# Performance work log

Measured on AMD Instinct MI355X. Metric: run time of the kernel, lower is better.

Reference implementation:

```python
import jax, jax.numpy as jnp
import numpy as np

N = 8192
D = 512


def setup_inputs() -> dict:
    key = jax.random.key(0)
    ks = jax.random.split(key, 7)
    X = jax.random.normal(ks[0], (N, D), dtype=jnp.float32)
    adj = jax.random.randint(ks[1], (N, N), 0, 2, dtype=jnp.int32)
    # guarantee at least one neighbor per row (self-loop) so softmax is defined
    adj = adj.at[jnp.arange(N), jnp.arange(N)].set(1)
    s = 1.0 / np.sqrt(D)
    Wq = jax.random.normal(ks[2], (D, D), dtype=jnp.float32) * s
    Wk = jax.random.normal(ks[3], (D, D), dtype=jnp.float32) * s
    Wv = jax.random.normal(ks[4], (D, D), dtype=jnp.float32) * s
    Wo = jax.random.normal(ks[5], (D, D), dtype=jnp.float32) * s
    bo = jnp.zeros((D,), dtype=jnp.float32)
    return {"X": X, "adj": adj, "Wq": Wq, "Wk": Wk, "Wv": Wv, "Wo": Wo, "bo": bo}


def reference(X, adj, Wq, Wk, Wv, Wo, bo):
    # torch Linear(no bias): y = x @ W.T
    Q = X @ Wq.T                                  # [N, D]
    K = X @ Wk.T                                  # [N, D]
    V = X @ Wv.T                                  # [N, D]
    scale = 1.0 / jnp.sqrt(jnp.asarray(D, X.dtype))
    scores = jnp.einsum('nd,md->nm', Q, K) * scale  # [N, N]
    scores = jnp.where(adj == 0, -jnp.inf, scores)
    attn = jax.nn.softmax(scores, axis=-1)          # [N, N]
    out = attn @ V                                  # [N, D]
    out = out @ Wo.T + bo                           # [N, D]
    return out
```

## Files before the change

### kernel.cpp

```cpp
#include <hip/hip_runtime.h>

namespace {

constexpr int NR = 8192;
constexpr int DD = 512;
constexpr int NSPLIT = 4;
constexpr int KVLEN = NR / NSPLIT;
constexpr int KT = 32;
constexpr int NT = KVLEN / KT;
constexpr int QB = 64;
constexpr float SCALE = 0.04419417382415922f;

typedef __bf16 bf16x8 __attribute__((ext_vector_type(8)));
typedef __bf16 bf16x4 __attribute__((ext_vector_type(4)));
typedef float  f32x16 __attribute__((ext_vector_type(16)));

__device__ __forceinline__ f32x16 mfma(bf16x8 a, bf16x8 b, f32x16 c) {
    return __builtin_amdgcn_mfma_f32_32x32x16_bf16(a, b, c, 0, 0, 0);
}

__device__ __forceinline__ size_t kfa(int n, int d) {
    size_t chunk = (size_t)(((n >> 5) * 4 + (d >> 7)) * 8 + ((d >> 4) & 7));
    return chunk * 512 + ((((d >> 3) & 1) * 32 + (n & 31)) * 8) + (d & 7);
}
__device__ __forceinline__ size_t vfa(int n, int d) {
    size_t chunk = (size_t)(((n >> 5) * 4 + (d >> 7)) * 8 +
                            ((d >> 6) & 1) * 4 + ((d >> 5) & 1) * 2 + ((n >> 4) & 1));
    return chunk * 512 + ((((n >> 3) & 1) * 32 + (d & 31)) * 8) + (n & 7);
}

__global__ void __launch_bounds__(256)
cast_kernel(const float* __restrict__ in, __bf16* __restrict__ out, int n8) {
    int i = blockIdx.x * 256 + threadIdx.x;
    if (i >= n8) return;
    const float4* p = (const float4*)(in + (size_t)i * 8);
    float4 v0 = p[0], v1 = p[1];
    bf16x8 o;
    o[0] = (__bf16)v0.x; o[1] = (__bf16)v0.y; o[2] = (__bf16)v0.z; o[3] = (__bf16)v0.w;
    o[4] = (__bf16)v1.x; o[5] = (__bf16)v1.y; o[6] = (__bf16)v1.z; o[7] = (__bf16)v1.w;
    *(bf16x8*)(out + (size_t)i * 8) = o;
}

__global__ void __launch_bounds__(256)
bitpack_kernel(const int* __restrict__ adj, unsigned long long* __restrict__ abits) {
    const int w = threadIdx.x >> 6, lane = threadIdx.x & 63;
    const int q = blockIdx.x * 4 + w;
    const int* row = adj + (size_t)q * NR;
    unsigned long long* orow = abits + (size_t)q * (NR / 64);
    for (int i = 0; i < NR / 64; ++i) {
        unsigned long long m = __ballot(row[i * 64 + lane] != 0);
        if (lane == 0) orow[i] = m;
    }
}

template<bool FINAL>
__global__ void __launch_bounds__(256, 2)
gemm_kernel(const __bf16* __restrict__ A, const __bf16* __restrict__ B0,
            const __bf16* __restrict__ B1, const __bf16* __restrict__ B2,
            __bf16* __restrict__ C0, __bf16* __restrict__ C1, __bf16* __restrict__ C2,
            const float* __restrict__ bias, float* __restrict__ Cf)
{
    const __bf16* B = B0;
    __bf16* Cb = C0;
    int mode = 0;
    if (!FINAL) {
        if (blockIdx.y == 1)      { B = B1; Cb = C1; mode = 1; }
        else if (blockIdx.y == 2) { B = B2; Cb = C2; mode = 2; }
    }
    __shared__ __bf16 As[128][72];
    __shared__ __bf16 Bs[128][72];
    const int t = threadIdx.x;
    const int w = t >> 6, lane = t & 63, lo = lane & 31, hi = lane >> 5;
    const int wm = w >> 1, wn = w & 1;
    const int bm = (blockIdx.x >> 2) * 128;
    const int bn = (blockIdx.x & 3) * 128;

    f32x16 acc[2][2];
    #pragma unroll
    for (int a = 0; a < 2; ++a)
        #pragma unroll
        for (int b = 0; b < 2; ++b)
            #pragma unroll
            for (int r = 0; r < 16; ++r) acc[a][b][r] = 0.f;

    for (int k0 = 0; k0 < DD; k0 += 64) {
        __syncthreads();
        #pragma unroll
        for (int pp = 0; pp < 2; ++pp) {
            int r = pp * 64 + (t >> 2), c = (t & 3) * 16;
            *(bf16x8*)&As[r][c]     = *(const bf16x8*)(A + (size_t)(bm + r) * DD + k0 + c);
            *(bf16x8*)&As[r][c + 8] = *(const bf16x8*)(A + (size_t)(bm + r) * DD + k0 + c + 8);
            *(bf16x8*)&Bs[r][c]     = *(const bf16x8*)(B + (size_t)(bn + r) * DD + k0 + c);
            *(bf16x8*)&Bs[r][c + 8] = *(const bf16x8*)(B + (size_t)(bn + r) * DD + k0 + c + 8);
        }
        __syncthreads();
        #pragma unroll
        for (int ks = 0; ks < 4; ++ks) {
            bf16x8 a0 = *(const bf16x8*)&As[wm * 64 + lo][ks * 16 + hi * 8];
            bf16x8 a1 = *(const bf16x8*)&As[wm * 64 + 32 + lo][ks * 16 + hi * 8];
            bf16x8 b0 = *(const bf16x8*)&Bs[wn * 64 + lo][ks * 16 + hi * 8];
            bf16x8 b1 = *(const bf16x8*)&Bs[wn * 64 + 32 + lo][ks * 16 + hi * 8];
            acc[0][0] = mfma(a0, b0, acc[0][0]);
            acc[0][1] = mfma(a0, b1, acc[0][1]);
            acc[1][0] = mfma(a1, b0, acc[1][0]);
            acc[1][1] = mfma(a1, b1, acc[1][1]);
        }
    }
    #pragma unroll
    for (int mi = 0; mi < 2; ++mi)
        #pragma unroll
        for (int ni = 0; ni < 2; ++ni) {
            int col = bn + wn * 64 + ni * 32 + lo;
            float bv = 0.f;
            if (FINAL) bv = bias[col];
            #pragma unroll
            for (int r = 0; r < 16; ++r) {
                int row = bm + wm * 64 + mi * 32 + (r & 3) + 8 * (r >> 2) + 4 * hi;
                if (FINAL) {
                    Cf[(size_t)row * DD + col] = acc[mi][ni][r] + bv;
                } else {
                    size_t a;
                    if (mode == 1)      a = kfa(row, col);
                    else if (mode == 2) a = vfa(row, col);
                    else                a = (size_t)row * DD + col;
                    Cb[a] = (__bf16)acc[mi][ni][r];
                }
            }
        }
}

__global__ void __launch_bounds__(256, 2)
flash_kernel(const __bf16* __restrict__ Qg, const __bf16* __restrict__ KF,
             const __bf16* __restrict__ VF, const unsigned long long* __restrict__ abits,
             __bf16* __restrict__ Opart, float* __restrict__ lsum_g)
{
    __shared__ __bf16 Sp[4][QB][40];
    __shared__ __bf16 Pl[QB][40];
    __shared__ float  ll[QB];

    const int t = threadIdx.x;
    const int w = t >> 6, lane = t & 63, lo = lane & 31, hi = lane >> 5;
    const int bid = blockIdx.x;
    const int xcd = bid & 7;
    const int split = xcd >> 1;
    const int qblk = (((xcd & 1) << 6) | (bid >> 3)) * QB;
    const int kv0 = split * KVLEN;

    bf16x8 qa[2][8];
    #pragma unroll
    for (int mi = 0; mi < 2; ++mi)
        #pragma unroll
        for (int ks = 0; ks < 8; ++ks)
            qa[mi][ks] = *(const bf16x8*)(Qg + (size_t)(qblk + mi * 32 + lo) * DD + w * 128 + ks * 16 + hi * 8);

    f32x16 O[2][2][2];
    #pragma unroll
    for (int h = 0; h < 2; ++h)
        #pragma unroll
        for (int a = 0; a < 2; ++a)
            #pragma unroll
            for (int b = 0; b < 2; ++b)
                #pragma unroll
                for (int r = 0; r < 16; ++r) O[h][a][b][r] = 0.f;

    const int qo = w * 16 + (lane >> 2);
    const int c8 = (lane & 3) * 8;
    const unsigned long long* abp = abits + (size_t)(qblk + qo) * (NR / 64) + kv0 / 64;
    unsigned long long acur = abp[0];
    unsigned long long anxt = abp[1];

    float l_run = 0.f;

    for (int tl = 0; tl < NT; ++tl) {
        if (tl && !(tl & 1)) {
            acur = anxt;
            int idx = (tl >> 1) + 1; if (idx > 31) idx = 31;
            anxt = abp[idx];
        }
        const int tile = (kv0 >> 5) + tl;
        const __bf16* kf = KF + (size_t)(tile * 4 + w) * 4096;

        f32x16 St0, St1;
        #pragma unroll
        for (int r = 0; r < 16; ++r) { St0[r] = 0.f; St1[r] = 0.f; }
        #pragma unroll
        for (int ks = 0; ks < 8; ++ks) {
            bf16x8 kb = *(const bf16x8*)(kf + ks * 512 + lane * 8);
            St0 = mfma(kb, qa[0][ks], St0);
            St1 = mfma(kb, qa[1][ks], St1);
        }
        #pragma unroll
        for (int g = 0; g < 4; ++g) {
            bf16x4 v0, v1;
            #pragma unroll
            for (int j = 0; j < 4; ++j) { v0[j] = (__bf16)St0[4 * g + j]; v1[j] = (__bf16)St1[4 * g + j]; }
            *(bf16x4*)&Sp[w][lo][8 * g + 4 * hi]      = v0;
            *(bf16x4*)&Sp[w][32 + lo][8 * g + 4 * hi] = v1;
        }
        __syncthreads();

        {
            bf16x8 p0 = *(const bf16x8*)&Sp[0][qo][c8];
            bf16x8 p1 = *(const bf16x8*)&Sp[1][qo][c8];
            bf16x8 p2 = *(const bf16x8*)&Sp[2][qo][c8];
            bf16x8 p3 = *(const bf16x8*)&Sp[3][qo][c8];
            unsigned m8 = ((unsigned)(acur >> ((tl & 1) << 5)) >> c8) & 0xffu;
            float lsum = 0.f;
            bf16x8 pb;
            #pragma unroll
            for (int i = 0; i < 8; ++i) {
                float v = ((float)p0[i] + (float)p1[i] + (float)p2[i] + (float)p3[i]) * SCALE;
                float pv = ((m8 >> i) & 1u) ? __expf(v) : 0.f;
                lsum += pv;
                pb[i] = (__bf16)pv;
            }
            lsum += __shfl_xor(lsum, 1);
            lsum += __shfl_xor(lsum, 2);
            l_run += lsum;
            *(bf16x8*)&Pl[qo][c8] = pb;
        }
        __syncthreads();

        bf16x8 pa[2][2];
        #pragma unroll
        for (int mi = 0; mi < 2; ++mi)
            #pragma unroll
            for (int ks = 0; ks < 2; ++ks)
                pa[mi][ks] = *(const bf16x8*)&Pl[mi * 32 + lo][ks * 16 + hi * 8];
        const __bf16* vf = VF + (size_t)(tile * 4 + w) * 4096;
        #pragma unroll
        for (int h = 0; h < 2; ++h)
            #pragma unroll
            for (int ni = 0; ni < 2; ++ni) {
                bf16x8 vb0 = *(const bf16x8*)(vf + (h * 4 + ni * 2 + 0) * 512 + lane * 8);
                bf16x8 vb1 = *(const bf16x8*)(vf + (h * 4 + ni * 2 + 1) * 512 + lane * 8);
                O[h][0][ni] = mfma(pa[0][0], vb0, O[h][0][ni]);
                O[h][1][ni] = mfma(pa[1][0], vb0, O[h][1][ni]);
                O[h][0][ni] = mfma(pa[0][1], vb1, O[h][0][ni]);
                O[h][1][ni] = mfma(pa[1][1], vb1, O[h][1][ni]);
            }
    }
    if ((lane & 3) == 0) {
        ll[qo] = l_run;
        lsum_g[(size_t)split * NR + qblk + qo] = l_run;
    }
    __syncthreads();
    #pragma unroll
    for (int mi = 0; mi < 2; ++mi)
        #pragma unroll
        for (int g = 0; g < 4; ++g) {
            float4 lv = *(const float4*)&ll[mi * 32 + 8 * g + 4 * hi];
            #pragma unroll
            for (int j = 0; j < 4; ++j) {
                float lval = (&lv.x)[j];
                float inv = (lval > 0.f) ? 1.f / lval : 0.f;
                int row = qblk + mi * 32 + 8 * g + 4 * hi + j;
                #pragma unroll
                for (int h = 0; h < 2; ++h)
                    #pragma unroll
                    for (int ni = 0; ni < 2; ++ni) {
                        int col = w * 128 + h * 64 + ni * 32 + lo;
                        Opart[(size_t)split * NR * DD + (size_t)row * DD + col] =
                            (__bf16)(O[h][mi][ni][g * 4 + j] * inv);
                    }
            }
        }
}

__global__ void __launch_bounds__(256)
merge_kernel(const __bf16* __restrict__ Opart, const float* __restrict__ lsum_g,
             __bf16* __restrict__ attn)
{
    int idx = blockIdx.x * 256 + threadIdx.x;
    int q = idx >> 6;
    int c = (idx & 63) * 8;
    float l0 = lsum_g[q], l1 = lsum_g[NR + q], l2 = lsum_g[2 * NR + q], l3 = lsum_g[3 * NR + q];
    float Winv = 1.f / (l0 + l1 + l2 + l3);
    float w0 = l0 * Winv, w1 = l1 * Winv, w2 = l2 * Winv, w3 = l3 * Winv;
    const size_t base = (size_t)q * DD + c;
    const size_t stride = (size_t)NR * DD;
    bf16x8 o0 = *(const bf16x8*)(Opart + base);
    bf16x8 o1 = *(const bf16x8*)(Opart + stride + base);
    bf16x8 o2 = *(const bf16x8*)(Opart + 2 * stride + base);
    bf16x8 o3 = *(const bf16x8*)(Opart + 3 * stride + base);
    bf16x8 o;
    #pragma unroll
    for (int i = 0; i < 8; ++i)
        o[i] = (__bf16)(w0 * (float)o0[i] + w1 * (float)o1[i] +
                        w2 * (float)o2[i] + w3 * (float)o3[i]);
    *(bf16x8*)(attn + base) = o;
}

}

extern "C" void kernel_launch(void* const* d_in, const int* in_sizes, int n_in,
                              void* d_out, int out_size, void* d_ws, size_t ws_size,
                              hipStream_t stream)
{
    (void)in_sizes; (void)n_in; (void)out_size; (void)ws_size;
    const float* X  = (const float*)d_in[0];
    const int*   adj = (const int*)d_in[1];
    const float* Wq = (const float*)d_in[2];
    const float* Wk = (const float*)d_in[3];
    const float* Wv = (const float*)d_in[4];
    const float* Wo = (const float*)d_in[5];
    const float* bo = (const float*)d_in[6];
    float* out = (float*)d_out;

    char* ws = (char*)d_ws;
    __bf16* Xb   = (__bf16*)(ws + 0);
    __bf16* Att  = (__bf16*)(ws + 0);
    __bf16* Wqb  = (__bf16*)(ws + 8388608);
    __bf16* Wkb  = (__bf16*)(ws + 8912896);
    __bf16* Wvb  = (__bf16*)(ws + 9437184);
    __bf16* Wob  = (__bf16*)(ws + 9961472);
    __bf16* Qb   = (__bf16*)(ws + 10485760);
    __bf16* KFb  = (__bf16*)(ws + 18874368);
    __bf16* VFb  = (__bf16*)(ws + 27262976);
    unsigned long long* abits = (unsigned long long*)(ws + 35651584);
    __bf16* Op   = (__bf16*)(ws + 44040192);
    float*  lseb = (float*)(ws + 77594624);

    bitpack_kernel<<<2048, 256, 0, stream>>>(adj, abits);
    cast_kernel<<<2048, 256, 0, stream>>>(X,  Xb,  NR * DD / 8);
    cast_kernel<<<128,  256, 0, stream>>>(Wq, Wqb, DD * DD / 8);
    cast_kernel<<<128,  256, 0, stream>>>(Wk, Wkb, DD * DD / 8);
    cast_kernel<<<128,  256, 0, stream>>>(Wv, Wvb, DD * DD / 8);
    cast_kernel<<<128,  256, 0, stream>>>(Wo, Wob, DD * DD / 8);

    gemm_kernel<false><<<dim3(256, 3), 256, 0, stream>>>(Xb, Wqb, Wkb, Wvb,
                                                         Qb, KFb, VFb, nullptr, nullptr);
    flash_kernel<<<512, 256, 0, stream>>>(Qb, KFb, VFb, abits, Op, lseb);
    merge_kernel<<<2048, 256, 0, stream>>>(Op, lseb, Att);
    gemm_kernel<true><<<dim3(256, 1), 256, 0, stream>>>(Att, Wob, nullptr, nullptr,
                                                        nullptr, nullptr, nullptr, bo, out);
}
```

Before: 459.8 us.

## Software-pipeline flash loop and repack V in a separate transpose kernel

```diff
diff --git a/kernel.cpp b/kernel.cpp
--- a/kernel.cpp
+++ b/kernel.cpp
@@ -65,7 +65,7 @@
     int mode = 0;
     if (!FINAL) {
         if (blockIdx.y == 1)      { B = B1; Cb = C1; mode = 1; }
-        else if (blockIdx.y == 2) { B = B2; Cb = C2; mode = 2; }
+        else if (blockIdx.y == 2) { B = B2; Cb = C2; }
     }
     __shared__ __bf16 As[128][72];
     __shared__ __bf16 Bs[128][72];
@@ -119,14 +119,35 @@
                 if (FINAL) {
                     Cf[(size_t)row * DD + col] = acc[mi][ni][r] + bv;
                 } else {
-                    size_t a;
-                    if (mode == 1)      a = kfa(row, col);
-                    else if (mode == 2) a = vfa(row, col);
-                    else                a = (size_t)row * DD + col;
+                    size_t a = (mode == 1) ? kfa(row, col) : ((size_t)row * DD + col);
                     Cb[a] = (__bf16)acc[mi][ni][r];
                 }
             }
         }
+}
+
+__global__ void __launch_bounds__(256)
+repack_v(const __bf16* __restrict__ V, __bf16* __restrict__ VF) {
+    __shared__ __bf16 tile[64][72];
+    const int t = threadIdx.x;
+    const int rb = blockIdx.x * 64;
+    const int cb = blockIdx.y * 64;
+    #pragma unroll
+    for (int pp = 0; pp < 2; ++pp) {
+        int r = pp * 32 + (t >> 3), c = (t & 7) * 8;
+        *(bf16x8*)&tile[r][c] = *(const bf16x8*)(V + (size_t)(rb + r) * DD + cb + c);
+    }
+    __syncthreads();
+    #pragma unroll
+    for (int pp = 0; pp < 2; ++pp) {
+        int vid = pp * 256 + t;
+        int oct = vid >> 6;
+        int dd = vid & 63;
+        bf16x8 o;
+        #pragma unroll
+        for (int e = 0; e < 8; ++e) o[e] = tile[oct * 8 + e][dd];
+        *(bf16x8*)(VF + vfa(rb + oct * 8, cb + dd)) = o;
+    }
 }
 
 __global__ void __launch_bounds__(256, 2)
@@ -170,16 +191,10 @@
     unsigned long long anxt = abp[1];
 
     float l_run = 0.f;
-
-    for (int tl = 0; tl < NT; ++tl) {
-        if (tl && !(tl & 1)) {
-            acur = anxt;
-            int idx = (tl >> 1) + 1; if (idx > 31) idx = 31;
-            anxt = abp[idx];
-        }
-        const int tile = (kv0 >> 5) + tl;
-        const __bf16* kf = KF + (size_t)(tile * 4 + w) * 4096;
-
+    const int tile0 = kv0 >> 5;
+
+    {
+        const __bf16* kf = KF + (size_t)(tile0 * 4 + w) * 4096;
         f32x16 St0, St1;
         #pragma unroll
         for (int r = 0; r < 16; ++r) { St0[r] = 0.f; St1[r] = 0.f; }
@@ -197,8 +212,77 @@
             *(bf16x4*)&Sp[w][lo][8 * g + 4 * hi]      = v0;
             *(bf16x4*)&Sp[w][32 + lo][8 * g + 4 * hi] = v1;
         }
+    }
+    __syncthreads();
+    {
+        bf16x8 p0 = *(const bf16x8*)&Sp[0][qo][c8];
+        bf16x8 p1 = *(const bf16x8*)&Sp[1][qo][c8];
+        bf16x8 p2 = *(const bf16x8*)&Sp[2][qo][c8];
+        bf16x8 p3 = *(const bf16x8*)&Sp[3][qo][c8];
+        unsigned m8 = ((unsigned)(acur >> 0) >> c8) & 0xffu;
+        float lsum = 0.f;
+        bf16x8 pb;
+        #pragma unroll
+        for (int i = 0; i < 8; ++i) {
+            float v = ((float)p0[i] + (float)p1[i] + (float)p2[i] + (float)p3[i]) * SCALE;
+            float pv = ((m8 >> i) & 1u) ? __expf(v) : 0.f;
+            lsum += pv;
+            pb[i] = (__bf16)pv;
+        }
+        lsum += __shfl_xor(lsum, 1);
+        lsum += __shfl_xor(lsum, 2);
+        l_run += lsum;
+        *(bf16x8*)&Pl[qo][c8] = pb;
+    }
+    __syncthreads();
+
+    for (int tl = 1; tl < NT; ++tl) {
+        if (!(tl & 1)) {
+            acur = anxt;
+            int idx = (tl >> 1) + 1; if (idx > 31) idx = 31;
+            anxt = abp[idx];
+        }
+        {
+            bf16x8 pa[2][2];
+            #pragma unroll
+            for (int mi = 0; mi < 2; ++mi)
+                #pragma unroll
+                for (int ks = 0; ks < 2; ++ks)
+                    pa[mi][ks] = *(const bf16x8*)&Pl[mi * 32 + lo][ks * 16 + hi * 8];
+            const __bf16* vf = VF + (size_t)((tile0 + tl - 1) * 4 + w) * 4096;
+            #pragma unroll
+            for (int h = 0; h < 2; ++h)
+                #pragma unroll
+                for (int ni = 0; ni < 2; ++ni) {
+                    bf16x8 vb0 = *(const bf16x8*)(vf + (h * 4 + ni * 2 + 0) * 512 + lane * 8);
+                    bf16x8 vb1 = *(const bf16x8*)(vf + (h * 4 + ni * 2 + 1) * 512 + lane * 8);
+                    O[h][0][ni] = mfma(pa[0][0], vb0, O[h][0][ni]);
+                    O[h][1][ni] = mfma(pa[1][0], vb0, O[h][1][ni]);
+                    O[h][0][ni] = mfma(pa[0][1], vb1, O[h][0][ni]);
+                    O[h][1][ni] = mfma(pa[1][1], vb1, O[h][1][ni]);
+                }
+        }
+        {
+            const __bf16* kf = KF + (size_t)((tile0 + tl) * 4 + w) * 4096;
+            f32x16 St0, St1;
+            #pragma unroll
+            for (int r = 0; r < 16; ++r) { St0[r] = 0.f; St1[r] = 0.f; }
+            #pragma unroll
+            for (int ks = 0; ks < 8; ++ks) {
+                bf16x8 kb = *(const bf16x8*)(kf + ks * 512 + lane * 8);
+                St0 = mfma(kb, qa[0][ks], St0);
+                St1 = mfma(kb, qa[1][ks], St1);
+            }
+            #pragma unroll
+            for (int g = 0; g < 4; ++g) {
+                bf16x4 v0, v1;
+                #pragma unroll
+                for (int j = 0; j < 4; ++j) { v0[j] = (__bf16)St0[4 * g + j]; v1[j] = (__bf16)St1[4 * g + j]; }
+                *(bf16x4*)&Sp[w][lo][8 * g + 4 * hi]      = v0;
+                *(bf16x4*)&Sp[w][32 + lo][8 * g + 4 * hi] = v1;
+            }
+        }
         __syncthreads();
-
         {
             bf16x8 p0 = *(const bf16x8*)&Sp[0][qo][c8];
             bf16x8 p1 = *(const bf16x8*)&Sp[1][qo][c8];
@@ -220,14 +304,15 @@
             *(bf16x8*)&Pl[qo][c8] = pb;
         }
         __syncthreads();
-
+    }
+    {
         bf16x8 pa[2][2];
         #pragma unroll
         for (int mi = 0; mi < 2; ++mi)
             #pragma unroll
             for (int ks = 0; ks < 2; ++ks)
                 pa[mi][ks] = *(const bf16x8*)&Pl[mi * 32 + lo][ks * 16 + hi * 8];
-        const __bf16* vf = VF + (size_t)(tile * 4 + w) * 4096;
+        const __bf16* vf = VF + (size_t)((tile0 + NT - 1) * 4 + w) * 4096;
         #pragma unroll
         for (int h = 0; h < 2; ++h)
             #pragma unroll
@@ -318,6 +403,7 @@
     __bf16* KFb  = (__bf16*)(ws + 18874368);
     __bf16* VFb  = (__bf16*)(ws + 27262976);
     unsigned long long* abits = (unsigned long long*)(ws + 35651584);
+    __bf16* Vb   = (__bf16*)(ws + 44040192);
     __bf16* Op   = (__bf16*)(ws + 44040192);
     float*  lseb = (float*)(ws + 77594624);
 
@@ -329,7 +415,8 @@
     cast_kernel<<<128,  256, 0, stream>>>(Wo, Wob, DD * DD / 8);
 
     gemm_kernel<false><<<dim3(256, 3), 256, 0, stream>>>(Xb, Wqb, Wkb, Wvb,
-                                                         Qb, KFb, VFb, nullptr, nullptr);
+                                                         Qb, KFb, Vb, nullptr, nullptr);
+    repack_v<<<dim3(128, 8), 256, 0, stream>>>(Vb, VFb);
     flash_kernel<<<512, 256, 0, stream>>>(Qb, KFb, VFb, abits, Op, lseb);
     merge_kernel<<<2048, 256, 0, stream>>>(Op, lseb, Att);
     gemm_kernel<true><<<dim3(256, 1), 256, 0, stream>>>(Att, Wob, nullptr, nullptr,
```

Result: faster. 447.2 us (-2.7%).

## Stage K tiles in LDS via async DMA and compute full-D scores per wave

Applied to the files above, without the earlier changes.

```diff
diff --git a/kernel.cpp b/kernel.cpp
--- a/kernel.cpp
+++ b/kernel.cpp
@@ -14,14 +14,25 @@
 typedef __bf16 bf16x8 __attribute__((ext_vector_type(8)));
 typedef __bf16 bf16x4 __attribute__((ext_vector_type(4)));
 typedef float  f32x16 __attribute__((ext_vector_type(16)));
-
-__device__ __forceinline__ f32x16 mfma(bf16x8 a, bf16x8 b, f32x16 c) {
+typedef float  f32x4  __attribute__((ext_vector_type(4)));
+
+__device__ __forceinline__ f32x16 mfma32(bf16x8 a, bf16x8 b, f32x16 c) {
     return __builtin_amdgcn_mfma_f32_32x32x16_bf16(a, b, c, 0, 0, 0);
 }
+__device__ __forceinline__ f32x4 mfma16(bf16x8 a, bf16x8 b, f32x4 c) {
+    return __builtin_amdgcn_mfma_f32_16x16x32_bf16(a, b, c, 0, 0, 0);
+}
+
+typedef const __attribute__((address_space(1))) void g_void;
+typedef __attribute__((address_space(3))) void l_void;
+__device__ __forceinline__ void lds_dma16(const void* g, void* l) {
+    __builtin_amdgcn_global_load_lds((g_void*)g, (l_void*)l, 16, 0, 0);
+}
 
 __device__ __forceinline__ size_t kfa(int n, int d) {
-    size_t chunk = (size_t)(((n >> 5) * 4 + (d >> 7)) * 8 + ((d >> 4) & 7));
-    return chunk * 512 + ((((d >> 3) & 1) * 32 + (n & 31)) * 8) + (d & 7);
+    int tile = n >> 5, kv = n & 31;
+    int chunk = (d >> 3) ^ (kv & 7);
+    return (size_t)tile * 16384 + kv * 512 + chunk * 8 + (d & 7);
 }
 __device__ __forceinline__ size_t vfa(int n, int d) {
     size_t chunk = (size_t)(((n >> 5) * 4 + (d >> 7)) * 8 +
@@ -42,14 +53,14 @@
 }
 
 __global__ void __launch_bounds__(256)
-bitpack_kernel(const int* __restrict__ adj, unsigned long long* __restrict__ abits) {
+bitpack_kernel(const int* __restrict__ adj, unsigned* __restrict__ abits) {
     const int w = threadIdx.x >> 6, lane = threadIdx.x & 63;
     const int q = blockIdx.x * 4 + w;
     const int* row = adj + (size_t)q * NR;
-    unsigned long long* orow = abits + (size_t)q * (NR / 64);
-    for (int i = 0; i < NR / 64; ++i) {
+    unsigned* orow = abits + (size_t)q * 256;
+    for (int i = 0; i < 128; ++i) {
         unsigned long long m = __ballot(row[i * 64 + lane] != 0);
-        if (lane == 0) orow[i] = m;
+        if (lane == 0) { orow[2 * i] = (unsigned)m; orow[2 * i + 1] = (unsigned)(m >> 32); }
     }
 }
 
@@ -65,7 +76,7 @@
     int mode = 0;
     if (!FINAL) {
         if (blockIdx.y == 1)      { B = B1; Cb = C1; mode = 1; }
-        else if (blockIdx.y == 2) { B = B2; Cb = C2; mode = 2; }
+        else if (blockIdx.y == 2) { B = B2; Cb = C2; }
     }
     __shared__ __bf16 As[128][72];
     __shared__ __bf16 Bs[128][72];
@@ -100,10 +111,10 @@
             bf16x8 a1 = *(const bf16x8*)&As[wm * 64 + 32 + lo][ks * 16 + hi * 8];
             bf16x8 b0 = *(const bf16x8*)&Bs[wn * 64 + lo][ks * 16 + hi * 8];
             bf16x8 b1 = *(const bf16x8*)&Bs[wn * 64 + 32 + lo][ks * 16 + hi * 8];
-            acc[0][0] = mfma(a0, b0, acc[0][0]);
-            acc[0][1] = mfma(a0, b1, acc[0][1]);
-            acc[1][0] = mfma(a1, b0, acc[1][0]);
-            acc[1][1] = mfma(a1, b1, acc[1][1]);
+            acc[0][0] = mfma32(a0, b0, acc[0][0]);
+            acc[0][1] = mfma32(a0, b1, acc[0][1]);
+            acc[1][0] = mfma32(a1, b0, acc[1][0]);
+            acc[1][1] = mfma32(a1, b1, acc[1][1]);
         }
     }
     #pragma unroll
@@ -119,39 +130,61 @@
                 if (FINAL) {
                     Cf[(size_t)row * DD + col] = acc[mi][ni][r] + bv;
                 } else {
-                    size_t a;
-                    if (mode == 1)      a = kfa(row, col);
-                    else if (mode == 2) a = vfa(row, col);
-                    else                a = (size_t)row * DD + col;
+                    size_t a = (mode == 1) ? kfa(row, col) : ((size_t)row * DD + col);
                     Cb[a] = (__bf16)acc[mi][ni][r];
                 }
             }
         }
 }
 
+__global__ void __launch_bounds__(256)
+repack_v(const __bf16* __restrict__ V, __bf16* __restrict__ VF) {
+    __shared__ __bf16 tile[64][72];
+    const int t = threadIdx.x;
+    const int rb = blockIdx.x * 64;
+    const int cb = blockIdx.y * 64;
+    #pragma unroll
+    for (int pp = 0; pp < 2; ++pp) {
+        int r = pp * 32 + (t >> 3), c = (t & 7) * 8;
+        *(bf16x8*)&tile[r][c] = *(const bf16x8*)(V + (size_t)(rb + r) * DD + cb + c);
+    }
+    __syncthreads();
+    #pragma unroll
+    for (int pp = 0; pp < 2; ++pp) {
+        int vid = pp * 256 + t;
+        int oct = vid >> 6;
+        int dd = vid & 63;
+        bf16x8 o;
+        #pragma unroll
+        for (int e = 0; e < 8; ++e) o[e] = tile[oct * 8 + e][dd];
+        *(bf16x8*)(VF + vfa(rb + oct * 8, cb + dd)) = o;
+    }
+}
+
 __global__ void __launch_bounds__(256, 2)
 flash_kernel(const __bf16* __restrict__ Qg, const __bf16* __restrict__ KF,
-             const __bf16* __restrict__ VF, const unsigned long long* __restrict__ abits,
+             const __bf16* __restrict__ VF, const unsigned* __restrict__ abits,
              __bf16* __restrict__ Opart, float* __restrict__ lsum_g)
 {
-    __shared__ __bf16 Sp[4][QB][40];
-    __shared__ __bf16 Pl[QB][40];
+    __shared__ __bf16 Klds[2][16384];
+    __shared__ __bf16 Pl[2][QB][40];
     __shared__ float  ll[QB];
 
     const int t = threadIdx.x;
-    const int w = t >> 6, lane = t & 63, lo = lane & 31, hi = lane >> 5;
+    const int w = t >> 6, lane = t & 63;
+    const int lo = lane & 31, hi = lane >> 5;
+    const int l15 = lane & 15, G = lane >> 4;
     const int bid = blockIdx.x;
     const int xcd = bid & 7;
     const int split = xcd >> 1;
     const int qblk = (((xcd & 1) << 6) | (bid >> 3)) * QB;
     const int kv0 = split * KVLEN;
-
-    bf16x8 qa[2][8];
-    #pragma unroll
-    for (int mi = 0; mi < 2; ++mi)
-        #pragma unroll
-        for (int ks = 0; ks < 8; ++ks)
-            qa[mi][ks] = *(const bf16x8*)(Qg + (size_t)(qblk + mi * 32 + lo) * DD + w * 128 + ks * 16 + hi * 8);
+    const int tile0 = kv0 >> 5;
+
+    bf16x8 qa[16];
+    #pragma unroll
+    for (int ks = 0; ks < 16; ++ks)
+        qa[ks] = *(const bf16x8*)(Qg + (size_t)(qblk + w * 16 + l15) * DD + ks * 32 + G * 8);
 
     f32x16 O[2][2][2];
     #pragma unroll
@@ -163,86 +196,84 @@
                 #pragma unroll
                 for (int r = 0; r < 16; ++r) O[h][a][b][r] = 0.f;
 
-    const int qo = w * 16 + (lane >> 2);
-    const int c8 = (lane & 3) * 8;
-    const unsigned long long* abp = abits + (size_t)(qblk + qo) * (NR / 64) + kv0 / 64;
-    unsigned long long acur = abp[0];
-    unsigned long long anxt = abp[1];
-
+    const unsigned* abp = abits + (size_t)(qblk + w * 16 + l15) * 256 + tile0;
+    unsigned wcur = abp[0];
     float l_run = 0.f;
+    const int hsw = l15 & 7;
+
+    #pragma unroll
+    for (int i = 0; i < 8; ++i)
+        lds_dma16(KF + (size_t)tile0 * 16384 + w * 4096 + i * 512 + lane * 8,
+                  &Klds[0][w * 4096 + i * 512]);
+    __syncthreads();
 
     for (int tl = 0; tl < NT; ++tl) {
-        if (tl && !(tl & 1)) {
-            acur = anxt;
-            int idx = (tl >> 1) + 1; if (idx > 31) idx = 31;
-            anxt = abp[idx];
-        }
-        const int tile = (kv0 >> 5) + tl;
-        const __bf16* kf = KF + (size_t)(tile * 4 + w) * 4096;
-
-        f32x16 St0, St1;
-        #pragma unroll
-        for (int r = 0; r < 16; ++r) { St0[r] = 0.f; St1[r] = 0.f; }
-        #pragma unroll
-        for (int ks = 0; ks < 8; ++ks) {
-            bf16x8 kb = *(const bf16x8*)(kf + ks * 512 + lane * 8);
-            St0 = mfma(kb, qa[0][ks], St0);
-            St1 = mfma(kb, qa[1][ks], St1);
-        }
-        #pragma unroll
-        for (int g = 0; g < 4; ++g) {
-            bf16x4 v0, v1;
-            #pragma unroll
-            for (int j = 0; j < 4; ++j) { v0[j] = (__bf16)St0[4 * g + j]; v1[j] = (__bf16)St1[4 * g + j]; }
-            *(bf16x4*)&Sp[w][lo][8 * g + 4 * hi]      = v0;
-            *(bf16x4*)&Sp[w][32 + lo][8 * g + 4 * hi] = v1;
-        }
-        __syncthreads();
-
+        const int b = tl & 1;
+        const int tn = (tl + 1 == NT) ? 0 : tl + 1;
+        #pragma unroll
+        for (int i = 0; i < 8; ++i)
+            lds_dma16(KF + (size_t)(tile0 + tn) * 16384 + w * 4096 + i * 512 + lane * 8,
+                      &Klds[b ^ 1][w * 4096 + i * 512]);
+        asm volatile("" ::: "memory");
+
+        f32x4 St0, St1;
+        #pragma unroll
+        for (int r = 0; r < 4; ++r) { St0[r] = 0.f; St1[r] = 0.f; }
+        #pragma unroll
+        for (int ks = 0; ks < 16; ++ks) {
+            int csw = (((ks * 4 + G) ^ hsw) << 3);
+            bf16x8 k0 = *(const bf16x8*)&Klds[b][l15 * 512 + csw];
+            bf16x8 k1 = *(const bf16x8*)&Klds[b][(16 + l15) * 512 + csw];
+            St0 = mfma16(k0, qa[ks], St0);
+            St1 = mfma16(k1, qa[ks], St1);
+        }
         {
-            bf16x8 p0 = *(const bf16x8*)&Sp[0][qo][c8];
-            bf16x8 p1 = *(const bf16x8*)&Sp[1][qo][c8];
-            bf16x8 p2 = *(const bf16x8*)&Sp[2][qo][c8];
-            bf16x8 p3 = *(const bf16x8*)&Sp[3][qo][c8];
-            unsigned m8 = ((unsigned)(acur >> ((tl & 1) << 5)) >> c8) & 0xffu;
-            float lsum = 0.f;
-            bf16x8 pb;
-            #pragma unroll
-            for (int i = 0; i < 8; ++i) {
-                float v = ((float)p0[i] + (float)p1[i] + (float)p2[i] + (float)p3[i]) * SCALE;
-                float pv = ((m8 >> i) & 1u) ? __expf(v) : 0.f;
-                lsum += pv;
-                pb[i] = (__bf16)pv;
+            float l_add = 0.f;
+            bf16x4 p0v, p1v;
+            #pragma unroll
+            for (int r = 0; r < 4; ++r) {
+                float s0 = St0[r] * SCALE;
+                float s1 = St1[r] * SCALE;
+                float pv0 = ((wcur >> (G * 4 + r)) & 1u) ? __expf(s0) : 0.f;
+                float pv1 = ((wcur >> (16 + G * 4 + r)) & 1u) ? __expf(s1) : 0.f;
+                l_add += pv0 + pv1;
+                p0v[r] = (__bf16)pv0;
+                p1v[r] = (__bf16)pv1;
             }
-            lsum += __shfl_xor(lsum, 1);
-            lsum += __shfl_xor(lsum, 2);
-            l_run += lsum;
-            *(bf16x8*)&Pl[qo][c8] = pb;
-        }
-        __syncthreads();
+            *(bf16x4*)&Pl[b][w * 16 + l15][G * 4]      = p0v;
+            *(bf16x4*)&Pl[b][w * 16 + l15][16 + G * 4] = p1v;
+            float a = l_add + __shfl_xor(l_add, 16);
+            a += __shfl_xor(a, 32);
+            l_run += a;
+        }
+        unsigned wnxt = abp[tn];
+
+        asm volatile("s_waitcnt vmcnt(1) lgkmcnt(0)" ::: "memory");
+        asm volatile("s_barrier" ::: "memory");
 
         bf16x8 pa[2][2];
         #pragma unroll
         for (int mi = 0; mi < 2; ++mi)
             #pragma unroll
-            for (int ks = 0; ks < 2; ++ks)
-                pa[mi][ks] = *(const bf16x8*)&Pl[mi * 32 + lo][ks * 16 + hi * 8];
-        const __bf16* vf = VF + (size_t)(tile * 4 + w) * 4096;
+            for (int ksp = 0; ksp < 2; ++ksp)
+                pa[mi][ksp] = *(const bf16x8*)&Pl[b][mi * 32 + lo][ksp * 16 + hi * 8];
+        const __bf16* vf = VF + (size_t)((tile0 + tl) * 4 + w) * 4096;
         #pragma unroll
         for (int h = 0; h < 2; ++h)
             #pragma unroll
             for (int ni = 0; ni < 2; ++ni) {
                 bf16x8 vb0 = *(const bf16x8*)(vf + (h * 4 + ni * 2 + 0) * 512 + lane * 8);
                 bf16x8 vb1 = *(const bf16x8*)(vf + (h * 4 + ni * 2 + 1) * 512 + lane * 8);
-                O[h][0][ni] = mfma(pa[0][0], vb0, O[h][0][ni]);
-                O[h][1][ni] = mfma(pa[1][0], vb0, O[h][1][ni]);
-                O[h][0][ni] = mfma(pa[0][1], vb1, O[h][0][ni]);
-                O[h][1][ni] = mfma(pa[1][1], vb1, O[h][1][ni]);
+                O[h][0][ni] = mfma32(pa[0][0], vb0, O[h][0][ni]);
+                O[h][1][ni] = mfma32(pa[1][0], vb0, O[h][1][ni]);
+                O[h][0][ni] = mfma32(pa[0][1], vb1, O[h][0][ni]);
+                O[h][1][ni] = mfma32(pa[1][1], vb1, O[h][1][ni]);
             }
-    }
-    if ((lane & 3) == 0) {
-        ll[qo] = l_run;
-        lsum_g[(size_t)split * NR + qblk + qo] = l_run;
+        wcur = wnxt;
+    }
+    if (lane < 16) {
+        ll[w * 16 + lane] = l_run;
+        lsum_g[(size_t)split * NR + qblk + w * 16 + lane] = l_run;
     }
     __syncthreads();
     #pragma unroll
@@ -317,7 +348,8 @@
     __bf16* Qb   = (__bf16*)(ws + 10485760);
     __bf16* KFb  = (__bf16*)(ws + 18874368);
     __bf16* VFb  = (__bf16*)(ws + 27262976);
-    unsigned long long* abits = (unsigned long long*)(ws + 35651584);
+    unsigned* abits = (unsigned*)(ws + 35651584);
+    __bf16* Vb   = (__bf16*)(ws + 44040192);
     __bf16* Op   = (__bf16*)(ws + 44040192);
     float*  lseb = (float*)(ws + 77594624);
 
@@ -329,7 +361,8 @@
     cast_kernel<<<128,  256, 0, stream>>>(Wo, Wob, DD * DD / 8);
 
     gemm_kernel<false><<<dim3(256, 3), 256, 0, stream>>>(Xb, Wqb, Wkb, Wvb,
-                                                         Qb, KFb, VFb, nullptr, nullptr);
+                                                         Qb, KFb, Vb, nullptr, nullptr);
+    repack_v<<<dim3(128, 8), 256, 0, stream>>>(Vb, VFb);
     flash_kernel<<<512, 256, 0, stream>>>(Qb, KFb, VFb, abits, Op, lseb);
     merge_kernel<<<2048, 256, 0, stream>>>(Op, lseb, Att);
     gemm_kernel<true><<<dim3(256, 1), 256, 0, stream>>>(Att, Wob, nullptr, nullptr,
```

Result: faster. 443.9 us (-3.4%).
